# Kernel tuning notes

Hardware: AMD Instinct MI355X
Metric: run time of the kernel (lower is better)

## Reference

```python
import jax, jax.numpy as jnp
import numpy as np

H = 512      # hidden_size (hardcoded in __init__)
WD = 1024    # word_dim (hardcoded)
V = 4096     # len(i2w)+4
B, S, T = 256, 80, 28


def setup_inputs() -> dict:
    key = jax.random.key(0)
    ks = jax.random.split(key, 14)

    def gl(k, shape, fan_in):
        return (jax.random.normal(k, shape, jnp.float32) / np.sqrt(fan_in)).astype(jnp.float32)

    return {
        "encoder_last_hidden_state": jax.random.normal(ks[0], (1, B, H), jnp.float32),
        "encoder_output": jax.random.normal(ks[1], (B, S, H), jnp.float32),
        "targets": jax.random.randint(ks[2], (B, T), 0, V, dtype=jnp.int32),
        # embedding table
        "embedding": gl(ks[3], (V, WD), WD),
        # attention MLP (4 stacked linears, no activations, per the source)
        "W1": gl(ks[4], (2 * H, H), 2 * H), "b1": jnp.zeros((H,), jnp.float32),
        "W2": gl(ks[5], (H, H), H), "b2": jnp.zeros((H,), jnp.float32),
        "W3": gl(ks[6], (H, H), H), "b3": jnp.zeros((H,), jnp.float32),
        "W4": gl(ks[7], (H, H), H), "b4": jnp.zeros((H,), jnp.float32),
        "Ww": gl(ks[8], (H, 1), H),
        # GRU (input = hidden_size + word_dim = 1536), PyTorch gate order r,z,n
        "W_ih": gl(ks[9], (3 * H, H + WD), H + WD), "b_ih": jnp.zeros((3 * H,), jnp.float32),
        "W_hh": gl(ks[10], (3 * H, H), H), "b_hh": jnp.zeros((3 * H,), jnp.float32),
        # output projection
        "Wo": gl(ks[11], (H, V), H), "bo": jnp.zeros((V,), jnp.float32),
    }


def reference(encoder_last_hidden_state, encoder_output, targets, embedding,
              W1, b1, W2, b2, W3, b3, W4, b4, Ww,
              W_ih, b_ih, W_hh, b_hh, Wo, bo):
    n_steps = targets.shape[1] - 1  # seq_len - 1 decode steps

    def attention(h, enc):
        # h: (B,H) decoder hidden; enc: (B,S,H)
        hs = jnp.broadcast_to(h[:, None, :], enc.shape)
        m = jnp.concatenate([enc, hs], axis=-1)          # (B,S,2H)
        x = m @ W1 + b1
        x = x @ W2 + b2
        x = x @ W3 + b3
        x = x @ W4 + b4
        attw = jax.nn.softmax((x @ Ww)[..., 0], axis=1)  # (B,S)
        return jnp.einsum('bs,bsh->bh', attw, enc)       # context (B,H)

    def gru_cell(x, h):
        gi = x @ W_ih.T + b_ih
        gh = h @ W_hh.T + b_hh
        ir, iz, inn = jnp.split(gi, 3, axis=-1)
        hr, hz, hn = jnp.split(gh, 3, axis=-1)
        r = jax.nn.sigmoid(ir + hr)
        z = jax.nn.sigmoid(iz + hz)
        n = jnp.tanh(inn + r * hn)
        return (1.0 - z) * n + z * h

    h0 = encoder_last_hidden_state[0]                    # (B,H)
    w0 = jnp.ones((encoder_output.shape[0],), jnp.int32) # <BOS> = 1

    def step(carry, _):
        h, w = carry
        emb = embedding[w]                               # (B,WD)
        ctx = attention(h, encoder_output)               # (B,H)
        x = jnp.concatenate([emb, ctx], axis=-1)         # (B,WD+H)
        hn = gru_cell(x, h)
        logits = hn @ Wo + bo                            # (B,V)
        wn = jnp.argmax(logits, axis=-1).astype(jnp.int32)
        return (hn, wn), logits

    _, logits_seq = jax.lax.scan(step, (h0, w0), None, length=n_steps)
    seq_logProb = jnp.swapaxes(logits_seq, 0, 1)         # (B, T-1, V)
    seq_predictions = jnp.argmax(seq_logProb, axis=-1)
    return seq_logProb, seq_predictions
```

## Files before the change

### kernel.cpp

```cpp
#include <hip/hip_runtime.h>

#define B_ 256
#define S_ 80
#define H_ 512
#define V_ 4096
#define NSTEP 27

typedef unsigned short u16;
typedef __attribute__((ext_vector_type(8))) short short8v;
typedef __attribute__((ext_vector_type(4))) float f32x4;
typedef __attribute__((ext_vector_type(4))) unsigned short ushort4v;

#define MFMA_(a,b,c) __builtin_amdgcn_mfma_f32_16x16x32_bf16(a,b,c,0,0,0)
#define MFMA3(acc, ah, al, bh, bl) do{ acc = MFMA_(ah,bh,acc); acc = MFMA_(ah,bl,acc); acc = MFMA_(al,bh,acc);}while(0)

__device__ __forceinline__ unsigned fkey(float v){
    unsigned u = __float_as_uint(v);
    return (u & 0x80000000u) ? ~u : (u | 0x80000000u);
}
__device__ __forceinline__ u16 bf16_rne(float f){
    unsigned u = __float_as_uint(f);
    return (u16)((u + 0x7FFFu + ((u >> 16) & 1u)) >> 16);
}
__device__ __forceinline__ void split_f4(float4 v, ushort4v& hi, ushort4v& lo){
    float arr[4] = {v.x, v.y, v.z, v.w};
    ushort4v h, l;
#pragma unroll
    for (int i = 0; i < 4; ++i){
        u16 hb = bf16_rne(arr[i]);
        h[i] = hb;
        l[i] = bf16_rne(arr[i] - __uint_as_float(((unsigned)hb) << 16));
    }
    hi = h; lo = l;
}

__global__ __launch_bounds__(64) void matvec512(const float* __restrict__ W,
                                                const float* __restrict__ v,
                                                float* __restrict__ out){
    int row = blockIdx.x, lane = threadIdx.x;
    const float* wr = W + row * 512;
    float s = 0.f;
#pragma unroll
    for (int i = 0; i < 8; ++i) s += wr[lane + 64*i] * v[lane + 64*i];
#pragma unroll
    for (int off = 32; off; off >>= 1) s += __shfl_xor(s, off);
    if (lane == 0) out[row] = s;
}

__global__ __launch_bounds__(256) void prep_all(
    const float* __restrict__ Whh, const float* __restrict__ Wo,
    const float* __restrict__ emb, const float* __restrict__ Wih,
    const float* __restrict__ elhs,
    u16* __restrict__ WhhHi, u16* __restrict__ WhhLo,
    u16* __restrict__ WoThi, u16* __restrict__ WoTlo,
    u16* __restrict__ EmbHi, u16* __restrict__ EmbLo,
    u16* __restrict__ WihLHi, u16* __restrict__ WihLLo,
    u16* __restrict__ Sh, u16* __restrict__ Sl,
    unsigned* __restrict__ zp, int nz)
{
    __shared__ float T[64][65];
    int b = blockIdx.x, tid = threadIdx.x;
    if (b < 768){
        int idx = (b*256 + tid)*4;
        float4 v = *(const float4*)&Whh[idx];
        ushort4v h,l; split_f4(v,h,l);
        *(ushort4v*)&WhhHi[idx]=h; *(ushort4v*)&WhhLo[idx]=l;
    } else if (b < 1280){
        int lb = b - 768;
        int k0 = (lb & 7)*64, n0 = (lb >> 3)*64;
#pragma unroll
        for (int i = 0; i < 16; ++i){
            int idx = tid + i*256;
            int kk = idx >> 6, nn = idx & 63;
            T[kk][nn] = Wo[(size_t)(k0+kk)*4096 + n0+nn];
        }
        __syncthreads();
#pragma unroll
        for (int i = 0; i < 16; ++i){
            int idx = tid + i*256;
            int nn = idx >> 6, kk = idx & 63;
            float v = T[kk][nn];
            u16 hi = bf16_rne(v);
            u16 lo = bf16_rne(v - __uint_as_float(((unsigned)hi) << 16));
            size_t o = (size_t)(n0+nn)*512 + k0+kk;
            WoThi[o] = hi; WoTlo[o] = lo;
        }
    } else if (b < 5376){
        int idx = ((b-1280)*256 + tid)*4;
        float4 v = *(const float4*)&emb[idx];
        ushort4v h,l; split_f4(v,h,l);
        *(ushort4v*)&EmbHi[idx]=h; *(ushort4v*)&EmbLo[idx]=l;
    } else if (b < 6912){
        int id = ((b-5376)*256 + tid)*4;
        int r = id >> 10, c = id & 1023;
        float4 v = *(const float4*)&Wih[(size_t)r*1536 + c];
        ushort4v h,l; split_f4(v,h,l);
        *(ushort4v*)&WihLHi[id]=h; *(ushort4v*)&WihLLo[id]=l;
    } else if (b < 7040){
        int idx = ((b-6912)*256 + tid)*4;
        float4 v = *(const float4*)&elhs[idx];
        ushort4v h,l; split_f4(v,h,l);
        *(ushort4v*)&Sh[idx]=h; *(ushort4v*)&Sl[idx]=l;
    } else {
        int i = ((b-7040)*256 + tid)*4;
        if (i < nz){ zp[i]=0u; zp[i+1]=0u; zp[i+2]=0u; zp[i+3]=0u; }
    }
}

__global__ __launch_bounds__(512) void attn_ctx(const float* __restrict__ enc,
                                                const float* __restrict__ weff,
                                                float* __restrict__ ctx){
    __shared__ float att[S_];
    int b = blockIdx.x, tid = threadIdx.x;
    int wv = tid >> 6, lane = tid & 63;
    float w8[8];
#pragma unroll
    for (int i = 0; i < 8; ++i) w8[i] = weff[lane + 64*i];
    const float* eb = enc + (size_t)b * (S_*H_);
    for (int s = wv; s < S_; s += 8){
        const float* e = eb + s*512;
        float acc = 0.f;
#pragma unroll
        for (int i = 0; i < 8; ++i) acc += e[lane + 64*i] * w8[i];
#pragma unroll
        for (int off = 32; off; off >>= 1) acc += __shfl_xor(acc, off);
        if (lane == 0) att[s] = acc;
    }
    __syncthreads();
    if (tid == 0){
        float mx = att[0];
        for (int s = 1; s < S_; ++s) mx = fmaxf(mx, att[s]);
        float sum = 0.f;
        for (int s = 0; s < S_; ++s){ float e = expf(att[s] - mx); att[s] = e; sum += e; }
        float inv = 1.f / sum;
        for (int s = 0; s < S_; ++s) att[s] *= inv;
    }
    __syncthreads();
    float a = 0.f;
    for (int s = 0; s < S_; ++s) a += att[s] * eb[s*512 + tid];
    ctx[b*512 + tid] = a;
}

__device__ __forceinline__ void step_mm_body(char* smem, int m0, int nt, int n_logits,
    const u16* __restrict__ Ahg, const u16* __restrict__ Alg,
    const u16* __restrict__ WoHi, const u16* __restrict__ WoLo,
    const u16* __restrict__ WhhHi, const u16* __restrict__ WhhLo,
    const float* __restrict__ bo,
    float* __restrict__ logits, unsigned long long* __restrict__ Pcur,
    float* __restrict__ gh_out)
{
    u16 (*Ah)[2048] = (u16(*)[2048])(smem);
    u16 (*Al)[2048] = (u16(*)[2048])(smem + 8192);
    u16 (*Bh)[2048] = (u16(*)[2048])(smem + 16384);
    u16 (*Bl)[2048] = (u16(*)[2048])(smem + 24576);
    bool isL = nt < n_logits;
    int nbase = (isL ? nt : nt - n_logits) * 64;
    const u16* Bhg = isL ? WoHi : WhhHi;
    const u16* Blg = isL ? WoLo : WhhLo;
    int tid = threadIdx.x, lane = tid & 63, wid = tid >> 6;
    int wy = wid & 1, wx = wid >> 1;
    int l15 = lane & 15, rg = lane >> 4, lk = rg * 8;
    int sr = tid >> 2, sk8 = (tid & 3) * 8;

    const u16* gAh = Ahg + (size_t)(m0 + sr)*512 + sk8;
    const u16* gAl = Alg + (size_t)(m0 + sr)*512 + sk8;
    const u16* gBh = Bhg + (size_t)(nbase + sr)*512 + sk8;
    const u16* gBl = Blg + (size_t)(nbase + sr)*512 + sk8;

    *(short8v*)&Ah[0][tid*8] = *(const short8v*)gAh;
    *(short8v*)&Al[0][tid*8] = *(const short8v*)gAl;
    *(short8v*)&Bh[0][tid*8] = *(const short8v*)gBh;
    *(short8v*)&Bl[0][tid*8] = *(const short8v*)gBl;
    short8v r1a = *(const short8v*)(gAh + 32), r1b = *(const short8v*)(gAl + 32);
    short8v r1c = *(const short8v*)(gBh + 32), r1d = *(const short8v*)(gBl + 32);
    short8v r2a = *(const short8v*)(gAh + 64), r2b = *(const short8v*)(gAl + 64);
    short8v r2c = *(const short8v*)(gBh + 64), r2d = *(const short8v*)(gBl + 64);
    __syncthreads();

    f32x4 acc[2][2] = {};
    int p = 0;
    for (int k0 = 0; k0 < 512; k0 += 32){
        if (k0 + 32 < 512){
            *(short8v*)&Ah[p^1][tid*8] = r1a;
            *(short8v*)&Al[p^1][tid*8] = r1b;
            *(short8v*)&Bh[p^1][tid*8] = r1c;
            *(short8v*)&Bl[p^1][tid*8] = r1d;
            r1a = r2a; r1b = r2b; r1c = r2c; r1d = r2d;
            if (k0 + 96 < 512){
                r2a = *(const short8v*)(gAh + k0 + 96);
                r2b = *(const short8v*)(gAl + k0 + 96);
                r2c = *(const short8v*)(gBh + k0 + 96);
                r2d = *(const short8v*)(gBl + k0 + 96);
            }
        }
        short8v afh0 = *(const short8v*)&Ah[p][(wy*32 +  0 + l15)*32 + lk];
        short8v afh1 = *(const short8v*)&Ah[p][(wy*32 + 16 + l15)*32 + lk];
        short8v afl0 = *(const short8v*)&Al[p][(wy*32 +  0 + l15)*32 + lk];
        short8v afl1 = *(const short8v*)&Al[p][(wy*32 + 16 + l15)*32 + lk];
        short8v bfh0 = *(const short8v*)&Bh[p][(wx*32 +  0 + l15)*32 + lk];
        short8v bfh1 = *(const short8v*)&Bh[p][(wx*32 + 16 + l15)*32 + lk];
        short8v bfl0 = *(const short8v*)&Bl[p][(wx*32 +  0 + l15)*32 + lk];
        short8v bfl1 = *(const short8v*)&Bl[p][(wx*32 + 16 + l15)*32 + lk];
        MFMA3(acc[0][0], afh0, afl0, bfh0, bfl0);
        MFMA3(acc[0][1], afh0, afl0, bfh1, bfl1);
        MFMA3(acc[1][0], afh1, afl1, bfh0, bfl0);
        MFMA3(acc[1][1], afh1, afl1, bfh1, bfl1);
        __syncthreads();
        p ^= 1;
    }

    int col0 = nbase + wx*32 + l15;
    if (isL){
        float bo0 = bo[col0], bo1 = bo[col0 + 16];
#pragma unroll
        for (int mf = 0; mf < 2; ++mf){
#pragma unroll
            for (int r = 0; r < 4; ++r){
                int row = m0 + wy*32 + mf*16 + rg*4 + r;
                float v0 = acc[mf][0][r] + bo0;
                float v1 = acc[mf][1][r] + bo1;
                float* crow = logits + (size_t)row * (NSTEP * (size_t)V_);
                crow[col0]      = v0;
                crow[col0 + 16] = v1;
                unsigned long long k0_ = ((unsigned long long)fkey(v0) << 32) | (unsigned)(4095 - col0);
                unsigned long long k1_ = ((unsigned long long)fkey(v1) << 32) | (unsigned)(4095 - (col0+16));
                unsigned long long best = k0_ > k1_ ? k0_ : k1_;
#pragma unroll
                for (int off = 1; off < 16; off <<= 1){
                    unsigned long long o = __shfl_xor(best, off);
                    if (o > best) best = o;
                }
                if (l15 == 0) atomicMax(&Pcur[row], best);
            }
        }
    } else {
#pragma unroll
        for (int mf = 0; mf < 2; ++mf)
#pragma unroll
            for (int r = 0; r < 4; ++r){
                int row = m0 + wy*32 + mf*16 + rg*4 + r;
                gh_out[(size_t)row*1536 + col0]      = acc[mf][0][r];
                gh_out[(size_t)row*1536 + col0 + 16] = acc[mf][1][r];
            }
    }
}

__global__ __launch_bounds__(256) void front3(
    const u16* __restrict__ EmbHi, const u16* __restrict__ EmbLo,
    const u16* __restrict__ WihLHi, const u16* __restrict__ WihLLo,
    float* __restrict__ Eproj,
    const float* __restrict__ ctx, const float* __restrict__ WihR,
    const float* __restrict__ bih, float* __restrict__ gictx,
    const u16* __restrict__ Sh0, const u16* __restrict__ Sl0,
    const u16* __restrict__ WhhHi, const u16* __restrict__ WhhLo,
    float* __restrict__ gh0)
{
    __shared__ __align__(16) char smem[32768];
    int b = blockIdx.x, tid = threadIdx.x;
    if (b < 384){
        int work = (b & 7) * 48 + (b >> 3);
        int bm = work / 12, bn = work % 12;
        int n0 = bn * 128, m0 = bm * 128;
        int lane = tid & 63, wid = tid >> 6;
        int wy = wid & 1, wx = wid >> 1;
        int l15 = lane & 15, rg = lane >> 4, lk = rg * 8;
        u16* Ah = (u16*)smem;
        u16* Al = (u16*)(smem + 8192);
        u16* Bh = (u16*)(smem + 16384);
        u16* Bl = (u16*)(smem + 24576);
        const u16* gA[2][2]; const u16* gB[2][2];
#pragma unroll
        for (int j = 0; j < 2; ++j){
            int s = tid + j*256;
            int row = s >> 2, k8 = (s & 3)*8;
            gA[0][j] = EmbHi + (size_t)(m0+row)*1024 + k8;
            gA[1][j] = EmbLo + (size_t)(m0+row)*1024 + k8;
            gB[0][j] = WihLHi + (size_t)(n0+row)*1024 + k8;
            gB[1][j] = WihLLo + (size_t)(n0+row)*1024 + k8;
        }
        short8v rA[2][2], rB[2][2];
#pragma unroll
        for (int h = 0; h < 2; ++h)
#pragma unroll
            for (int j = 0; j < 2; ++j){
                rA[h][j] = *(const short8v*)gA[h][j];
                rB[h][j] = *(const short8v*)gB[h][j];
            }
        f32x4 acc[4][4] = {};
        for (int k0 = 0; k0 < 1024; k0 += 32){
            __syncthreads();
#pragma unroll
            for (int j = 0; j < 2; ++j){
                int s8 = (tid + j*256)*8;
                *(short8v*)&Ah[s8] = rA[0][j];
                *(short8v*)&Al[s8] = rA[1][j];
                *(short8v*)&Bh[s8] = rB[0][j];
                *(short8v*)&Bl[s8] = rB[1][j];
            }
            __syncthreads();
            if (k0 + 32 < 1024){
#pragma unroll
                for (int h = 0; h < 2; ++h)
#pragma unroll
                    for (int j = 0; j < 2; ++j){
                        rA[h][j] = *(const short8v*)(gA[h][j] + k0 + 32);
                        rB[h][j] = *(const short8v*)(gB[h][j] + k0 + 32);
                    }
            }
            short8v afh[4], afl[4];
#pragma unroll
            for (int mf = 0; mf < 4; ++mf){
                afh[mf] = *(const short8v*)&Ah[(wy*64 + mf*16 + l15)*32 + lk];
                afl[mf] = *(const short8v*)&Al[(wy*64 + mf*16 + l15)*32 + lk];
            }
#pragma unroll
            for (int nf = 0; nf < 4; ++nf){
                short8v bfh = *(const short8v*)&Bh[(wx*64 + nf*16 + l15)*32 + lk];
                short8v bfl = *(const short8v*)&Bl[(wx*64 + nf*16 + l15)*32 + lk];
#pragma unroll
                for (int mf = 0; mf < 4; ++mf)
                    MFMA3(acc[mf][nf], afh[mf], afl[mf], bfh, bfl);
            }
        }
        int col0 = n0 + wx*64 + l15;
#pragma unroll
        for (int mf = 0; mf < 4; ++mf)
#pragma unroll
            for (int r = 0; r < 4; ++r){
                int row = m0 + wy*64 + mf*16 + rg*4 + r;
#pragma unroll
                for (int nf = 0; nf < 4; ++nf)
                    Eproj[(size_t)row*1536 + col0 + nf*16] = acc[mf][nf][r];
            }
    } else if (b < 576){
        int lb = b - 384;
        int m0 = (lb & 7) * 32, n0 = (lb >> 3) * 64;
        float (*As)[36] = (float(*)[36])smem;
        float (*Bs)[68] = (float(*)[68])(smem + 2304);
        int lk = tid & 15, lr = tid >> 4;
        int tx = tid & 15, ty = tid >> 4;
        float c[2][4] = {};
        for (int k0 = 0; k0 < 512; k0 += 16){
#pragma unroll
            for (int i = 0; i < 2; ++i)
                As[lk][lr*2 + i] = ctx[(size_t)(m0 + lr*2 + i)*512 + k0 + lk];
#pragma unroll
            for (int i = 0; i < 4; ++i)
                Bs[lk][lr*4 + i] = WihR[(size_t)(n0 + lr*4 + i)*1536 + k0 + lk];
            __syncthreads();
#pragma unroll
            for (int k = 0; k < 16; ++k){
                float b4[4];
                *(float4*)b4 = *(const float4*)&Bs[k][tx*4];
#pragma unroll
                for (int i = 0; i < 2; ++i){
                    float a = As[k][ty*2 + i];
#pragma unroll
                    for (int j = 0; j < 4; ++j) c[i][j] += a * b4[j];
                }
            }
            __syncthreads();
        }
#pragma unroll
        for (int j = 0; j < 4; ++j){
            float bb = bih[n0 + tx*4 + j];
#pragma unroll
            for (int i = 0; i < 2; ++i)
                gictx[(size_t)(m0 + ty*2 + i)*1536 + n0 + tx*4 + j] = c[i][j] + bb;
        }
    } else {
        int lb = b - 576;
        step_mm_body(smem, (lb & 3)*64, lb >> 2, 0,
                     Sh0, Sl0, nullptr, nullptr, WhhHi, WhhLo,
                     nullptr, nullptr, nullptr, gh0);
    }
}

__global__ __launch_bounds__(128) void gru_pointwise(
    const float* __restrict__ gh, const float* __restrict__ Eproj,
    const float* __restrict__ gictx, const float* __restrict__ bhh,
    const float* __restrict__ hprev, float* __restrict__ hnext,
    u16* __restrict__ Sh, u16* __restrict__ Sl,
    const unsigned long long* __restrict__ Pprev,
    float* __restrict__ preds, int t)
{
    int tid = threadIdx.x;
    int row = blockIdx.x;
    int jj = tid * 4;
    int w = 1;
    if (t > 0){
        w = 4095 - (int)(Pprev[row] & 0xFFFFFFFFull);
        if (w < 0) w = 0; if (w > 4095) w = 4095;
        if (tid == 0) preds[row*NSTEP + (t-1)] = (float)w;
    }
    const float* gr = gh + (size_t)row * 1536;
    const float* ep = Eproj + (size_t)w * 1536;
    const float* gc = gictx + (size_t)row * 1536;
    float4 g0 = *(const float4*)&gr[jj];
    float4 g1 = *(const float4*)&gr[512 + jj];
    float4 g2 = *(const float4*)&gr[1024 + jj];
    float4 e0 = *(const float4*)&ep[jj];
    float4 e1 = *(const float4*)&ep[512 + jj];
    float4 e2 = *(const float4*)&ep[1024 + jj];
    float4 c0 = *(const float4*)&gc[jj];
    float4 c1 = *(const float4*)&gc[512 + jj];
    float4 c2 = *(const float4*)&gc[1024 + jj];
    float4 b0 = *(const float4*)&bhh[jj];
    float4 b1 = *(const float4*)&bhh[512 + jj];
    float4 b2 = *(const float4*)&bhh[1024 + jj];
    float4 ho = *(const float4*)&hprev[(size_t)row*512 + jj];
    const float* G0 = (const float*)&g0; const float* G1 = (const float*)&g1;
    const float* G2 = (const float*)&g2;
    const float* E0 = (const float*)&e0; const float* E1 = (const float*)&e1;
    const float* E2 = (const float*)&e2;
    const float* C0 = (const float*)&c0; const float* C1 = (const float*)&c1;
    const float* C2 = (const float*)&c2;
    const float* B0 = (const float*)&b0; const float* B1 = (const float*)&b1;
    const float* B2 = (const float*)&b2;
    const float* HO = (const float*)&ho;
    float4 res;
    float* R = (float*)&res;
#pragma unroll
    for (int i = 0; i < 4; ++i){
        float gir = E0[i] + C0[i] + G0[i] + B0[i];
        float giz = E1[i] + C1[i] + G1[i] + B1[i];
        float gin = E2[i] + C2[i];
        float rr = 1.f / (1.f + expf(-gir));
        float zz = 1.f / (1.f + expf(-giz));
        float nn = tanhf(gin + rr * (G2[i] + B2[i]));
        R[i] = (1.f - zz)*nn + zz*HO[i];
    }
    size_t o = (size_t)row*512 + jj;
    *(float4*)&hnext[o] = res;
    ushort4v h4, l4; split_f4(res, h4, l4);
    *(ushort4v*)&Sh[o] = h4;
    *(ushort4v*)&Sl[o] = l4;
}

__global__ __launch_bounds__(256) void step_mm(
    const u16* __restrict__ Ahg, const u16* __restrict__ Alg,
    const u16* __restrict__ WoHi, const u16* __restrict__ WoLo,
    const u16* __restrict__ WhhHi, const u16* __restrict__ WhhLo,
    const float* __restrict__ bo,
    float* __restrict__ logits, unsigned long long* __restrict__ Pcur,
    float* __restrict__ gh_out, int n_logits)
{
    __shared__ __align__(16) char smem[32768];
    int bid = blockIdx.x;
    int work = (bid & 7) * 44 + (bid >> 3);
    step_mm_body(smem, (work & 3) * 64, work >> 2, n_logits,
                 Ahg, Alg, WoHi, WoLo, WhhHi, WhhLo, bo, logits, Pcur, gh_out);
}

__global__ __launch_bounds__(256) void final_pred(const unsigned long long* __restrict__ P,
                                                  float* __restrict__ preds){
    int b = threadIdx.x;
    int w = 4095 - (int)(P[b] & 0xFFFFFFFFull);
    if (w < 0) w = 0; if (w > 4095) w = 4095;
    preds[b*NSTEP + (NSTEP-1)] = (float)w;
}

extern "C" void kernel_launch(void* const* d_in, const int* in_sizes, int n_in,
                              void* d_out, int out_size, void* d_ws, size_t ws_size,
                              hipStream_t stream){
    const float* elhs = (const float*)d_in[0];
    const float* enc  = (const float*)d_in[1];
    const float* emb  = (const float*)d_in[3];
    const float* W1   = (const float*)d_in[4];
    const float* W2   = (const float*)d_in[6];
    const float* W3   = (const float*)d_in[8];
    const float* W4   = (const float*)d_in[10];
    const float* Ww   = (const float*)d_in[12];
    const float* Wih  = (const float*)d_in[13];
    const float* bih  = (const float*)d_in[14];
    const float* Whh  = (const float*)d_in[15];
    const float* bhh  = (const float*)d_in[16];
    const float* Wo   = (const float*)d_in[17];
    const float* bo   = (const float*)d_in[18];

    float* out = (float*)d_out;
    float* preds = out + (size_t)B_ * NSTEP * V_;

    float* ws = (float*)d_ws;
    float* Eproj  = ws;  ws += (size_t)V_ * 1536;
    float* gictx  = ws;  ws += (size_t)B_ * 1536;
    float* ctx    = ws;  ws += B_ * H_;
    float* t1     = ws;  ws += 512;
    float* t2     = ws;  ws += 512;
    float* weff   = ws;  ws += 512;
    float* Hf     = ws;  ws += 2 * B_ * H_;
    float* ghbuf  = ws;  ws += B_ * 1536;
    u16* WoT_hi = (u16*)ws;  ws += (size_t)V_ * 512 / 2;
    u16* WoT_lo = (u16*)ws;  ws += (size_t)V_ * 512 / 2;
    u16* WhhHi  = (u16*)ws;  ws += 1536 * 512 / 2;
    u16* WhhLo  = (u16*)ws;  ws += 1536 * 512 / 2;
    u16* Sh     = (u16*)ws;  ws += B_ * H_ / 2;
    u16* Sl     = (u16*)ws;  ws += B_ * H_ / 2;
    unsigned long long* P = (unsigned long long*)ws;

    u16* EmbHi  = (u16*)d_out;
    u16* EmbLo  = EmbHi + (size_t)V_*1024;
    u16* WihLHi = EmbLo + (size_t)V_*1024;
    u16* WihLLo = WihLHi + (size_t)1536*1024;

    prep_all<<<7054, 256, 0, stream>>>(Whh, Wo, emb, Wih, elhs,
                                       WhhHi, WhhLo, WoT_hi, WoT_lo,
                                       EmbHi, EmbLo, WihLHi, WihLLo,
                                       Sh, Sl, (unsigned*)P, NSTEP*256*2);
    matvec512<<<512, 64, 0, stream>>>(W4, Ww, t1);
    matvec512<<<512, 64, 0, stream>>>(W3, t1, t2);
    matvec512<<<512, 64, 0, stream>>>(W2, t2, t1);
    matvec512<<<512, 64, 0, stream>>>(W1, t1, weff);
    attn_ctx<<<B_, 512, 0, stream>>>(enc, weff, ctx);
    front3<<<672, 256, 0, stream>>>(EmbHi, EmbLo, WihLHi, WihLLo, Eproj,
                                    ctx, Wih + 1024, bih, gictx,
                                    Sh, Sl, WhhHi, WhhLo, ghbuf);

    for (int t = 0; t < NSTEP; ++t){
        const float* hr = (t == 0) ? elhs : (Hf + (size_t)((t-1) & 1) * (B_*H_));
        float*       hw = Hf + (size_t)(t & 1) * (B_*H_);
        const unsigned long long* Pprev = P + (size_t)(t > 0 ? t-1 : 0) * 256;
        gru_pointwise<<<256, 128, 0, stream>>>(ghbuf, Eproj, gictx, bhh, hr, hw,
                                               Sh, Sl, Pprev, preds, t);
        step_mm<<<352, 256, 0, stream>>>(Sh, Sl, WoT_hi, WoT_lo, WhhHi, WhhLo, bo,
                                         out + (size_t)t * V_, P + (size_t)t*256, ghbuf, 64);
    }
    final_pred<<<1, 256, 0, stream>>>(P + (size_t)(NSTEP-1)*256, preds);
}
```

Before: 701.7 us.

## Retile per-step GEMM to 32x64 blocks with register-prefetched double buffering

```diff
diff --git a/kernel.cpp b/kernel.cpp
--- a/kernel.cpp
+++ b/kernel.cpp
@@ -445,11 +445,94 @@
     float* __restrict__ logits, unsigned long long* __restrict__ Pcur,
     float* __restrict__ gh_out, int n_logits)
 {
-    __shared__ __align__(16) char smem[32768];
+    __shared__ __align__(16) char smem[24576];
+    u16 (*Ah)[1024] = (u16(*)[1024])(smem);
+    u16 (*Al)[1024] = (u16(*)[1024])(smem + 4096);
+    u16 (*Bh)[2048] = (u16(*)[2048])(smem + 8192);
+    u16 (*Bl)[2048] = (u16(*)[2048])(smem + 16384);
     int bid = blockIdx.x;
-    int work = (bid & 7) * 44 + (bid >> 3);
-    step_mm_body(smem, (work & 3) * 64, work >> 2, n_logits,
-                 Ahg, Alg, WoHi, WoLo, WhhHi, WhhLo, bo, logits, Pcur, gh_out);
+    int work = (bid & 7) * 88 + (bid >> 3);
+    int m0 = (work & 7) * 32;
+    int nt = work >> 3;
+    bool isL = nt < n_logits;
+    int nbase = (isL ? nt : nt - n_logits) * 64;
+    const u16* Bhg = isL ? WoHi : WhhHi;
+    const u16* Blg = isL ? WoLo : WhhLo;
+    int tid = threadIdx.x, lane = tid & 63, wid = tid >> 6;
+    int wy = wid & 1, wx = wid >> 1;
+    int l15 = lane & 15, rg = lane >> 4, lk = rg * 8;
+
+    int ahalf = tid >> 7, ai = tid & 127;
+    int ar = ai >> 2, ak8 = (ai & 3) * 8;
+    const u16* gA = (ahalf ? Alg : Ahg) + (size_t)(m0 + ar)*512 + ak8;
+    u16 (*Adst)[1024] = ahalf ? Al : Ah;
+    int br = tid >> 2, bk8 = (tid & 3) * 8;
+    const u16* gBh = Bhg + (size_t)(nbase + br)*512 + bk8;
+    const u16* gBl = Blg + (size_t)(nbase + br)*512 + bk8;
+
+    *(short8v*)&Adst[0][ai*8] = *(const short8v*)gA;
+    *(short8v*)&Bh[0][tid*8] = *(const short8v*)gBh;
+    *(short8v*)&Bl[0][tid*8] = *(const short8v*)gBl;
+    short8v a1 = *(const short8v*)(gA + 32),  a2 = *(const short8v*)(gA + 64);
+    short8v h1 = *(const short8v*)(gBh + 32), h2 = *(const short8v*)(gBh + 64);
+    short8v l1 = *(const short8v*)(gBl + 32), l2 = *(const short8v*)(gBl + 64);
+    __syncthreads();
+
+    f32x4 acc[2] = {};
+    int p = 0;
+    for (int k0 = 0; k0 < 512; k0 += 32){
+        if (k0 + 32 < 512){
+            *(short8v*)&Adst[p^1][ai*8] = a1;
+            *(short8v*)&Bh[p^1][tid*8] = h1;
+            *(short8v*)&Bl[p^1][tid*8] = l1;
+            a1 = a2; h1 = h2; l1 = l2;
+            if (k0 + 96 < 512){
+                a2 = *(const short8v*)(gA + k0 + 96);
+                h2 = *(const short8v*)(gBh + k0 + 96);
+                l2 = *(const short8v*)(gBl + k0 + 96);
+            }
+        }
+        short8v afh = *(const short8v*)&Ah[p][(wy*16 + l15)*32 + lk];
+        short8v afl = *(const short8v*)&Al[p][(wy*16 + l15)*32 + lk];
+        short8v bfh0 = *(const short8v*)&Bh[p][(wx*32 +  0 + l15)*32 + lk];
+        short8v bfh1 = *(const short8v*)&Bh[p][(wx*32 + 16 + l15)*32 + lk];
+        short8v bfl0 = *(const short8v*)&Bl[p][(wx*32 +  0 + l15)*32 + lk];
+        short8v bfl1 = *(const short8v*)&Bl[p][(wx*32 + 16 + l15)*32 + lk];
+        MFMA3(acc[0], afh, afl, bfh0, bfl0);
+        MFMA3(acc[1], afh, afl, bfh1, bfl1);
+        __syncthreads();
+        p ^= 1;
+    }
+
+    int col0 = nbase + wx*32 + l15;
+    if (isL){
+        float bo0 = bo[col0], bo1 = bo[col0 + 16];
+#pragma unroll
+        for (int r = 0; r < 4; ++r){
+            int row = m0 + wy*16 + rg*4 + r;
+            float v0 = acc[0][r] + bo0;
+            float v1 = acc[1][r] + bo1;
+            float* crow = logits + (size_t)row * (NSTEP * (size_t)V_);
+            crow[col0]      = v0;
+            crow[col0 + 16] = v1;
+            unsigned long long k0_ = ((unsigned long long)fkey(v0) << 32) | (unsigned)(4095 - col0);
+            unsigned long long k1_ = ((unsigned long long)fkey(v1) << 32) | (unsigned)(4095 - (col0+16));
+            unsigned long long best = k0_ > k1_ ? k0_ : k1_;
+#pragma unroll
+            for (int off = 1; off < 16; off <<= 1){
+                unsigned long long o = __shfl_xor(best, off);
+                if (o > best) best = o;
+            }
+            if (l15 == 0) atomicMax(&Pcur[row], best);
+        }
+    } else {
+#pragma unroll
+        for (int r = 0; r < 4; ++r){
+            int row = m0 + wy*16 + rg*4 + r;
+            gh_out[(size_t)row*1536 + col0]      = acc[0][r];
+            gh_out[(size_t)row*1536 + col0 + 16] = acc[1][r];
+        }
+    }
 }
 
 __global__ __launch_bounds__(256) void final_pred(const unsigned long long* __restrict__ P,
@@ -522,7 +605,7 @@
         const unsigned long long* Pprev = P + (size_t)(t > 0 ? t-1 : 0) * 256;
         gru_pointwise<<<256, 128, 0, stream>>>(ghbuf, Eproj, gictx, bhh, hr, hw,
                                                Sh, Sl, Pprev, preds, t);
-        step_mm<<<352, 256, 0, stream>>>(Sh, Sl, WoT_hi, WoT_lo, WhhHi, WhhLo, bo,
+        step_mm<<<704, 256, 0, stream>>>(Sh, Sl, WoT_hi, WoT_lo, WhhHi, WhhLo, bo,
                                          out + (size_t)t * V_, P + (size_t)t*256, ghbuf, 64);
     }
     final_pred<<<1, 256, 0, stream>>>(P + (size_t)(NSTEP-1)*256, preds);
```

After: 693.0 us. No clear change (-1.2%).
